# Performance work log

Hardware: AMD Instinct MI355X
Metric: run time of the kernel (lower is better)

## Reference

```python
import jax, jax.numpy as jnp
import numpy as np

N_NODES = 100000
N_EDGES = 1600000
HIDDEN = 128
MAX_DEG = 64
EPS = 1e-6


def setup_inputs() -> dict:
    key = jax.random.key(0)
    ks = jax.random.split(key, 6)
    x = jax.random.randint(ks[0], (N_NODES,), 0, MAX_DEG + 1)
    edge_index = jax.random.randint(ks[1], (2, N_EDGES), 0, N_NODES)
    edge_weight = jax.random.uniform(ks[2], (N_EDGES,), dtype=jnp.float32)
    emb = jax.random.normal(ks[3], (MAX_DEG + 1, HIDDEN), dtype=jnp.float32)
    # 5 GraphNorms in application order: emb_gn, conv0.gn, gns[0], conv1.gn, gns[1]
    gn_weight = jax.random.uniform(ks[4], (5, HIDDEN), dtype=jnp.float32)
    gn_bias = jnp.zeros((5, HIDDEN), dtype=jnp.float32)
    gn_mean_scale = jax.random.uniform(ks[5], (5, HIDDEN), dtype=jnp.float32)
    return {"x": x, "edge_index": edge_index, "edge_weight": edge_weight,
            "emb": emb, "gn_weight": gn_weight, "gn_bias": gn_bias,
            "gn_mean_scale": gn_mean_scale}


def _graphnorm(h, w, b, ms):
    # GLASS GraphNorm over the whole node set (single-graph batch)
    mean = jnp.mean(h, axis=0)              # [D]
    out = h - mean * ms                     # [N,D]
    std = jnp.sqrt(jnp.mean(out * out, axis=0) + EPS)
    return w * out / std + b


def reference(x, edge_index, edge_weight, emb, gn_weight, gn_bias, gn_mean_scale):
    row, col = edge_index[0], edge_index[1]
    n = N_NODES
    # mean-aggregated normalized adjacency (buildAdj, aggr='mean')
    deg = jax.ops.segment_sum(edge_weight, row, num_segments=n)
    deg = jnp.where(deg < 0.5, deg + 1.0, deg)
    w_norm = edge_weight / deg[row]         # [E]

    def spmm(h):
        # (adj @ h)[i] = sum_{e: row[e]=i} w_norm[e] * h[col[e]]
        return jax.ops.segment_sum(h[col] * w_norm[:, None], row, num_segments=n)

    # input embedding + emb_gn (dropout is identity in eval mode)
    h = emb[x]                              # [N, HIDDEN]
    h = _graphnorm(h, gn_weight[0], gn_bias[0], gn_mean_scale[0])
    # layer 0: GLASSConv (adj @ h -> gn) then outer gns[0] and ReLU
    h = spmm(h)
    h = _graphnorm(h, gn_weight[1], gn_bias[1], gn_mean_scale[1])
    h = _graphnorm(h, gn_weight[2], gn_bias[2], gn_mean_scale[2])
    h = jax.nn.relu(h)
    # layer 1 (last conv) then final gns[-1]; jk=False -> take last
    h = spmm(h)
    h = _graphnorm(h, gn_weight[3], gn_bias[3], gn_mean_scale[3])
    h = _graphnorm(h, gn_weight[4], gn_bias[4], gn_mean_scale[4])
    return h
```

## Files before the change

kernel.cpp:

```cpp
#include <hip/hip_runtime.h>

#define HID 128
#define EPSF 1e-6f

__device__ inline unsigned f2bf(float f) {
  unsigned u = __float_as_uint(f);
  return (u + 0x7fffu + ((u >> 16) & 1u)) >> 16;
}

__global__ void k_hist(const int* __restrict__ x, int n, int* __restrict__ hist) {
  __shared__ int lh[65];
  int t = threadIdx.x;
  if (t < 65) lh[t] = 0;
  __syncthreads();
  for (int i = blockIdx.x * blockDim.x + t; i < n; i += gridDim.x * blockDim.x)
    atomicAdd(&lh[x[i]], 1);
  __syncthreads();
  if (t < 65 && lh[t]) atomicAdd(&hist[t], lh[t]);
}

__global__ void k_cnt(const int* __restrict__ row, int e, int* __restrict__ cnt) {
  for (int i = blockIdx.x * blockDim.x + threadIdx.x; i < e; i += gridDim.x * blockDim.x)
    atomicAdd(&cnt[row[i]], 1);
}

__global__ void k_scan_partial(const int* __restrict__ cnt, int n, int* __restrict__ bsum) {
  __shared__ int sh[256];
  int t = threadIdx.x;
  int base = blockIdx.x * 2048 + t * 8;
  int s = 0;
#pragma unroll
  for (int j = 0; j < 8; ++j) { int idx = base + j; if (idx < n) s += cnt[idx]; }
  sh[t] = s; __syncthreads();
  for (int off = 128; off > 0; off >>= 1) {
    if (t < off) sh[t] += sh[t + off];
    __syncthreads();
  }
  if (t == 0) bsum[blockIdx.x] = sh[0];
}

__global__ void k_scan_bsum(int* __restrict__ bsum, int nb) {
  if (threadIdx.x == 0 && blockIdx.x == 0) {
    int acc = 0;
    for (int i = 0; i < nb; ++i) { int v = bsum[i]; bsum[i] = acc; acc += v; }
  }
}

__global__ void k_scan_final(const int* __restrict__ cnt, int n, const int* __restrict__ bsum,
                             int* __restrict__ rowptr, int* __restrict__ cursor) {
  __shared__ int sh[256];
  int t = threadIdx.x;
  int base = blockIdx.x * 2048 + t * 8;
  int v[8]; int s = 0;
#pragma unroll
  for (int j = 0; j < 8; ++j) { int idx = base + j; v[j] = (idx < n) ? cnt[idx] : 0; s += v[j]; }
  sh[t] = s; __syncthreads();
  for (int off = 1; off < 256; off <<= 1) {
    int val = (t >= off) ? sh[t - off] : 0;
    __syncthreads();
    sh[t] += val;
    __syncthreads();
  }
  int off0 = bsum[blockIdx.x] + sh[t] - s;
#pragma unroll
  for (int j = 0; j < 8; ++j) {
    int idx = base + j;
    if (idx < n) { rowptr[idx] = off0; cursor[idx] = off0; off0 += v[j]; }
  }
}

__global__ void k_scatter(const int* __restrict__ row, const int* __restrict__ col,
                          const float* __restrict__ ew, const int* __restrict__ x, int e,
                          int* __restrict__ cursor, int2* __restrict__ sedge) {
  for (int i = blockIdx.x * blockDim.x + threadIdx.x; i < e; i += gridDim.x * blockDim.x) {
    int r = row[i];
    int c = col[i];
    int xc = x[c];
    int pos = atomicAdd(&cursor[r], 1);
    sedge[pos] = make_int2(c | (xc << 17), __float_as_int(ew[i]));
  }
}

__global__ void k_gn0(const float* __restrict__ emb, const int* __restrict__ hist,
                      const float* __restrict__ gw, const float* __restrict__ gb,
                      const float* __restrict__ gms, float invN,
                      float* __restrict__ emb1) {
  int d = threadIdx.x;
  float s = 0.f, s2 = 0.f;
  for (int k = 0; k < 65; ++k) {
    float v = emb[k * HID + d];
    float c = (float)hist[k];
    s += c * v; s2 += c * v * v;
  }
  float m = s * invN, E2 = s2 * invN;
  float ms0 = gms[d], w0 = gw[d], b0 = gb[d];
  float sh = m * ms0;
  float a = w0 / sqrtf(E2 - 2.f * sh * m + sh * sh + EPSF);
  float c = b0 - a * sh;
  for (int k = 0; k < 65; ++k) emb1[k * HID + d] = fmaf(a, emb[k * HID + d], c);
}

__global__ void k_gnchain(const float* __restrict__ gsum, const float* __restrict__ gsq,
                          float invN, const float* __restrict__ gw, const float* __restrict__ gb,
                          const float* __restrict__ gms, int i1, int i2,
                          float* __restrict__ A, float* __restrict__ C) {
  int d = threadIdx.x;
  float m = gsum[d] * invN, E2 = gsq[d] * invN;
  float ms1 = gms[i1 * HID + d], w1 = gw[i1 * HID + d], b1 = gb[i1 * HID + d];
  float sh1 = m * ms1;
  float a1 = w1 / sqrtf(E2 - 2.f * sh1 * m + sh1 * sh1 + EPSF);
  float c1 = b1 - a1 * sh1;
  float m2 = a1 * m + c1;
  float E2b = a1 * a1 * E2 + 2.f * a1 * c1 * m + c1 * c1;
  float ms2 = gms[i2 * HID + d], w2 = gw[i2 * HID + d], b2 = gb[i2 * HID + d];
  float sh2 = m2 * ms2;
  float a2 = w2 / sqrtf(E2b - 2.f * sh2 * m2 + sh2 * sh2 + EPSF);
  float c2 = b2 - a2 * sh2;
  A[d] = a2 * a1;
  C[d] = a2 * c1 + c2;
}

__global__ __launch_bounds__(256) void k_spmm1(
    const int* __restrict__ rowptr, const int2* __restrict__ sedge,
    const float* __restrict__ emb1, int n, int nwaves,
    unsigned* __restrict__ h2b, float* __restrict__ gsum, float* __restrict__ gsq) {
  __shared__ float lemb[65 * HID];
  __shared__ float red[2][4][64][2];
  int t = threadIdx.x;
  for (int i = t; i < 65 * HID; i += 256) lemb[i] = emb1[i];
  __syncthreads();
  int l = t & 63, wv = t >> 6;
  int gwid = blockIdx.x * 4 + wv;
  float ps0 = 0, ps1 = 0, q0 = 0, q1 = 0;
  for (int node = gwid; node < n; node += nwaves) {
    int nd = __builtin_amdgcn_readfirstlane(node);
    int p0 = rowptr[nd], p1 = rowptr[nd + 1];
    float wsum = 0.f, a0 = 0.f, a1 = 0.f;
    int p = p0;
    int nfull = p0 + ((p1 - p0) & ~7);
    for (; p < nfull; p += 8) {
      int2 b[8];
#pragma unroll
      for (int k = 0; k < 8; ++k) b[k] = sedge[p + k];
#pragma unroll
      for (int k = 0; k < 8; ++k) {
        int xc = b[k].x >> 17;
        float w = __int_as_float(b[k].y);
        const float2 v = *(const float2*)&lemb[xc * HID + l * 2];
        wsum += w;
        a0 = fmaf(w, v.x, a0);
        a1 = fmaf(w, v.y, a1);
      }
    }
    for (; p < p1; ++p) {
      int2 b = sedge[p];
      int xc = b.x >> 17;
      float w = __int_as_float(b.y);
      const float2 v = *(const float2*)&lemb[xc * HID + l * 2];
      wsum += w;
      a0 = fmaf(w, v.x, a0);
      a1 = fmaf(w, v.y, a1);
    }
    float d = (wsum < 0.5f) ? wsum + 1.0f : wsum;
    float invd = 1.0f / d;
    a0 *= invd; a1 *= invd;
    h2b[(size_t)node * (HID / 2) + l] = f2bf(a0) | (f2bf(a1) << 16);
    ps0 += a0; ps1 += a1; q0 += a0 * a0; q1 += a1 * a1;
  }
  red[0][wv][l][0] = ps0; red[0][wv][l][1] = ps1;
  red[1][wv][l][0] = q0;  red[1][wv][l][1] = q1;
  __syncthreads();
  if (wv == 0) {
    float s0 = 0, s1 = 0, t0 = 0, t1 = 0;
#pragma unroll
    for (int k = 0; k < 4; ++k) {
      s0 += red[0][k][l][0]; s1 += red[0][k][l][1];
      t0 += red[1][k][l][0]; t1 += red[1][k][l][1];
    }
    atomicAdd(&gsum[l * 2], s0); atomicAdd(&gsum[l * 2 + 1], s1);
    atomicAdd(&gsq[l * 2], t0);  atomicAdd(&gsq[l * 2 + 1], t1);
  }
}

__global__ __launch_bounds__(256) void k_spmm2(
    const int* __restrict__ rowptr, const int2* __restrict__ sedge,
    const unsigned* __restrict__ h2b,
    const float* __restrict__ A, const float* __restrict__ C,
    int n, int nwaves, float* __restrict__ out,
    float* __restrict__ gsum, float* __restrict__ gsq) {
  __shared__ float red[2][4][64][2];
  int t = threadIdx.x;
  int l = t & 63, wv = t >> 6;
  int gwid = blockIdx.x * 4 + wv;
  float A0 = A[l * 2], A1 = A[l * 2 + 1], C0 = C[l * 2], C1 = C[l * 2 + 1];
  float ps0 = 0, ps1 = 0, q0 = 0, q1 = 0;
  for (int node = gwid; node < n; node += nwaves) {
    int nd = __builtin_amdgcn_readfirstlane(node);
    int p0 = rowptr[nd], p1 = rowptr[nd + 1];
    float wsum = 0.f, a0 = 0.f, a1 = 0.f;
    int cntf = (p1 - p0) >> 3;
    int p = p0;
    int2 b[8], nb[8];
    if (cntf) {
#pragma unroll
      for (int k = 0; k < 8; ++k) b[k] = sedge[p + k];
    }
    for (int it = 0; it < cntf; ++it) {
      unsigned u[8];
#pragma unroll
      for (int k = 0; k < 8; ++k) {
        int c = b[k].x & 0x1FFFF;
        u[k] = h2b[(size_t)c * (HID / 2) + l];
      }
      p += 8;
      if (it + 1 < cntf) {
#pragma unroll
        for (int k = 0; k < 8; ++k) nb[k] = sedge[p + k];
      }
#pragma unroll
      for (int k = 0; k < 8; ++k) {
        float w = __int_as_float(b[k].y);
        wsum += w;
        float h0 = __uint_as_float(u[k] << 16);
        float h1 = __uint_as_float(u[k] & 0xFFFF0000u);
        a0 = fmaf(w, fmaxf(fmaf(A0, h0, C0), 0.f), a0);
        a1 = fmaf(w, fmaxf(fmaf(A1, h1, C1), 0.f), a1);
      }
#pragma unroll
      for (int k = 0; k < 8; ++k) b[k] = nb[k];
    }
    for (; p < p1; ++p) {
      int2 e = sedge[p];
      int c = e.x & 0x1FFFF;
      unsigned uu = h2b[(size_t)c * (HID / 2) + l];
      float w = __int_as_float(e.y);
      wsum += w;
      float h0 = __uint_as_float(uu << 16);
      float h1 = __uint_as_float(uu & 0xFFFF0000u);
      a0 = fmaf(w, fmaxf(fmaf(A0, h0, C0), 0.f), a0);
      a1 = fmaf(w, fmaxf(fmaf(A1, h1, C1), 0.f), a1);
    }
    float d = (wsum < 0.5f) ? wsum + 1.0f : wsum;
    float invd = 1.0f / d;
    a0 *= invd; a1 *= invd;
    *(float2*)&out[(size_t)node * HID + l * 2] = make_float2(a0, a1);
    ps0 += a0; ps1 += a1; q0 += a0 * a0; q1 += a1 * a1;
  }
  red[0][wv][l][0] = ps0; red[0][wv][l][1] = ps1;
  red[1][wv][l][0] = q0;  red[1][wv][l][1] = q1;
  __syncthreads();
  if (wv == 0) {
    float s0 = 0, s1 = 0, t0 = 0, t1 = 0;
#pragma unroll
    for (int k = 0; k < 4; ++k) {
      s0 += red[0][k][l][0]; s1 += red[0][k][l][1];
      t0 += red[1][k][l][0]; t1 += red[1][k][l][1];
    }
    atomicAdd(&gsum[l * 2], s0); atomicAdd(&gsum[l * 2 + 1], s1);
    atomicAdd(&gsq[l * 2], t0);  atomicAdd(&gsq[l * 2 + 1], t1);
  }
}

__global__ void k_final(float* __restrict__ out, const float* __restrict__ A,
                        const float* __restrict__ C, int n) {
  __shared__ float la[HID], lc[HID];
  if (threadIdx.x < HID) { la[threadIdx.x] = A[threadIdx.x]; lc[threadIdx.x] = C[threadIdx.x]; }
  __syncthreads();
  int total = n * 32;
  for (int i = blockIdx.x * blockDim.x + threadIdx.x; i < total; i += gridDim.x * blockDim.x) {
    float4 v = *(float4*)(out + (size_t)i * 4);
    int cg = (i & 31) * 4;
    v.x = fmaf(la[cg + 0], v.x, lc[cg + 0]);
    v.y = fmaf(la[cg + 1], v.y, lc[cg + 1]);
    v.z = fmaf(la[cg + 2], v.z, lc[cg + 2]);
    v.w = fmaf(la[cg + 3], v.w, lc[cg + 3]);
    *(float4*)(out + (size_t)i * 4) = v;
  }
}

extern "C" void kernel_launch(void* const* d_in, const int* in_sizes, int n_in,
                              void* d_out, int out_size, void* d_ws, size_t ws_size,
                              hipStream_t stream) {
  const int* x = (const int*)d_in[0];
  const int* ei = (const int*)d_in[1];
  const float* ew = (const float*)d_in[2];
  const float* emb = (const float*)d_in[3];
  const float* gw = (const float*)d_in[4];
  const float* gb = (const float*)d_in[5];
  const float* gms = (const float*)d_in[6];
  float* out = (float*)d_out;

  const int n = in_sizes[0];
  const int e = in_sizes[1] / 2;
  const int* row = ei;
  const int* col = ei + e;

  float* wsf = (float*)d_ws;
  size_t o = 0;
  auto alloc = [&](size_t elems) -> size_t { size_t r = o; o += ((elems + 31) & ~(size_t)31); return r; };
  size_t cnt_o = alloc(n + 1);
  size_t hist_o = alloc(65);
  size_t sum2_o = alloc(HID), sq2_o = alloc(HID), sum4_o = alloc(HID), sq4_o = alloc(HID);
  size_t zero_end = o;
  size_t A12_o = alloc(HID), C12_o = alloc(HID), A34_o = alloc(HID), C34_o = alloc(HID);
  size_t rowptr_o = alloc(n + 1);
  size_t cursor_o = alloc(n + 1);
  size_t bsum_o = alloc(64);
  size_t emb1_o = alloc(65 * HID);
  size_t sedge_o = alloc((size_t)e * 2);
  size_t h2b_o = alloc((size_t)n * HID / 2);

  int* cnt = (int*)(wsf + cnt_o);
  int* hist = (int*)(wsf + hist_o);
  float* sum2 = wsf + sum2_o; float* sq2 = wsf + sq2_o;
  float* sum4 = wsf + sum4_o; float* sq4 = wsf + sq4_o;
  float* A12 = wsf + A12_o; float* C12 = wsf + C12_o;
  float* A34 = wsf + A34_o; float* C34 = wsf + C34_o;
  int* rowptr = (int*)(wsf + rowptr_o);
  int* cursor = (int*)(wsf + cursor_o);
  int* bsum = (int*)(wsf + bsum_o);
  float* emb1 = wsf + emb1_o;
  int2* sedge = (int2*)(wsf + sedge_o);
  unsigned* h2b = (unsigned*)(wsf + h2b_o);

  const float invN = 1.0f / (float)n;
  const int nblk = 2048;
  const int nwaves = nblk * 4;

  hipMemsetAsync(d_ws, 0, zero_end * sizeof(float), stream);
  k_hist<<<256, 256, 0, stream>>>(x, n, hist);
  k_cnt<<<2048, 256, 0, stream>>>(row, e, cnt);
  int nb = (n + 1 + 2047) / 2048;
  k_scan_partial<<<nb, 256, 0, stream>>>(cnt, n + 1, bsum);
  k_scan_bsum<<<1, 64, 0, stream>>>(bsum, nb);
  k_scan_final<<<nb, 256, 0, stream>>>(cnt, n + 1, bsum, rowptr, cursor);
  k_scatter<<<2048, 256, 0, stream>>>(row, col, ew, x, e, cursor, sedge);
  k_gn0<<<1, HID, 0, stream>>>(emb, hist, gw, gb, gms, invN, emb1);
  k_spmm1<<<nblk, 256, 0, stream>>>(rowptr, sedge, emb1, n, nwaves, h2b, sum2, sq2);
  k_gnchain<<<1, HID, 0, stream>>>(sum2, sq2, invN, gw, gb, gms, 1, 2, A12, C12);
  k_spmm2<<<nblk, 256, 0, stream>>>(rowptr, sedge, h2b, A12, C12, n, nwaves, out, sum4, sq4);
  k_gnchain<<<1, HID, 0, stream>>>(sum4, sq4, invN, gw, gb, gms, 3, 4, A34, C34);
  k_final<<<2048, 256, 0, stream>>>(out, A34, C34, n);
}
```

Baseline: 567.9 us.

## Software-pipeline SpMM gathers, bf16 embedding table, fuse hist/count, unroll scatter

Merges the histogram and row-count kernels into one launch. The edge scatter is unrolled by four so several independent loads and atomics are in flight per thread. The normalised embedding table is stored as packed bf16 in global memory instead of fp32 in LDS, which drops the per-block 33KB LDS fill and raises occupancy but adds rounding error to layer 0. Both SpMM kernels get a double-buffered pipeline over 8-edge chunks, prefetch of the next node's rowptr, a vectorised remainder path, and a launch_bounds occupancy hint, at the cost of higher register pressure.

```diff
diff --git a/kernel.cpp b/kernel.cpp
--- a/kernel.cpp
+++ b/kernel.cpp
@@ -8,20 +8,17 @@
   return (u + 0x7fffu + ((u >> 16) & 1u)) >> 16;
 }
 
-__global__ void k_hist(const int* __restrict__ x, int n, int* __restrict__ hist) {
+__global__ void k_histcnt(const int* __restrict__ x, int n, const int* __restrict__ row,
+                          int e, int* __restrict__ hist, int* __restrict__ cnt) {
   __shared__ int lh[65];
   int t = threadIdx.x;
   if (t < 65) lh[t] = 0;
   __syncthreads();
-  for (int i = blockIdx.x * blockDim.x + t; i < n; i += gridDim.x * blockDim.x)
-    atomicAdd(&lh[x[i]], 1);
+  int tid = blockIdx.x * blockDim.x + t, stride = gridDim.x * blockDim.x;
+  for (int i = tid; i < e; i += stride) atomicAdd(&cnt[row[i]], 1);
+  for (int i = tid; i < n; i += stride) atomicAdd(&lh[x[i]], 1);
   __syncthreads();
   if (t < 65 && lh[t]) atomicAdd(&hist[t], lh[t]);
-}
-
-__global__ void k_cnt(const int* __restrict__ row, int e, int* __restrict__ cnt) {
-  for (int i = blockIdx.x * blockDim.x + threadIdx.x; i < e; i += gridDim.x * blockDim.x)
-    atomicAdd(&cnt[row[i]], 1);
 }
 
 __global__ void k_scan_partial(const int* __restrict__ cnt, int n, int* __restrict__ bsum) {
@@ -69,35 +66,53 @@
   }
 }
 
-__global__ void k_scatter(const int* __restrict__ row, const int* __restrict__ col,
-                          const float* __restrict__ ew, const int* __restrict__ x, int e,
-                          int* __restrict__ cursor, int2* __restrict__ sedge) {
-  for (int i = blockIdx.x * blockDim.x + threadIdx.x; i < e; i += gridDim.x * blockDim.x) {
-    int r = row[i];
-    int c = col[i];
-    int xc = x[c];
-    int pos = atomicAdd(&cursor[r], 1);
-    sedge[pos] = make_int2(c | (xc << 17), __float_as_int(ew[i]));
+__global__ __launch_bounds__(256) void k_scatter(
+    const int* __restrict__ row, const int* __restrict__ col,
+    const float* __restrict__ ew, const int* __restrict__ x, int e,
+    int* __restrict__ cursor, int2* __restrict__ sedge) {
+  int tid = blockIdx.x * blockDim.x + threadIdx.x;
+  int stride = gridDim.x * blockDim.x;
+  for (int i0 = tid; i0 < e; i0 += stride * 4) {
+    int r[4], c[4], xc[4], idx[4]; float w[4]; bool valid[4];
+#pragma unroll
+    for (int k = 0; k < 4; ++k) {
+      int i = i0 + k * stride; valid[k] = (i < e);
+      if (valid[k]) { r[k] = row[i]; c[k] = col[i]; w[k] = ew[i]; }
+    }
+#pragma unroll
+    for (int k = 0; k < 4; ++k) if (valid[k]) xc[k] = x[c[k]];
+#pragma unroll
+    for (int k = 0; k < 4; ++k) if (valid[k]) idx[k] = atomicAdd(&cursor[r[k]], 1);
+#pragma unroll
+    for (int k = 0; k < 4; ++k)
+      if (valid[k]) sedge[idx[k]] = make_int2(c[k] | (xc[k] << 17), __float_as_int(w[k]));
   }
 }
 
 __global__ void k_gn0(const float* __restrict__ emb, const int* __restrict__ hist,
                       const float* __restrict__ gw, const float* __restrict__ gb,
                       const float* __restrict__ gms, float invN,
-                      float* __restrict__ emb1) {
-  int d = threadIdx.x;
-  float s = 0.f, s2 = 0.f;
+                      unsigned* __restrict__ emb1b) {
+  int t = threadIdx.x;
+  int d0 = t * 2, d1 = t * 2 + 1;
+  float s0 = 0, s20 = 0, s1 = 0, s21 = 0;
   for (int k = 0; k < 65; ++k) {
-    float v = emb[k * HID + d];
     float c = (float)hist[k];
-    s += c * v; s2 += c * v * v;
-  }
-  float m = s * invN, E2 = s2 * invN;
-  float ms0 = gms[d], w0 = gw[d], b0 = gb[d];
-  float sh = m * ms0;
-  float a = w0 / sqrtf(E2 - 2.f * sh * m + sh * sh + EPSF);
-  float c = b0 - a * sh;
-  for (int k = 0; k < 65; ++k) emb1[k * HID + d] = fmaf(a, emb[k * HID + d], c);
+    float v0 = emb[k * HID + d0], v1 = emb[k * HID + d1];
+    s0 += c * v0; s20 += c * v0 * v0;
+    s1 += c * v1; s21 += c * v1 * v1;
+  }
+  float m0 = s0 * invN, E20 = s20 * invN;
+  float m1 = s1 * invN, E21 = s21 * invN;
+  float sh0 = m0 * gms[d0], sh1 = m1 * gms[d1];
+  float aa0 = gw[d0] / sqrtf(E20 - 2.f * sh0 * m0 + sh0 * sh0 + EPSF);
+  float aa1 = gw[d1] / sqrtf(E21 - 2.f * sh1 * m1 + sh1 * sh1 + EPSF);
+  float cc0 = gb[d0] - aa0 * sh0, cc1 = gb[d1] - aa1 * sh1;
+  for (int k = 0; k < 65; ++k) {
+    float y0 = fmaf(aa0, emb[k * HID + d0], cc0);
+    float y1 = fmaf(aa1, emb[k * HID + d1], cc1);
+    emb1b[k * (HID / 2) + t] = f2bf(y0) | (f2bf(y1) << 16);
+  }
 }
 
 __global__ void k_gnchain(const float* __restrict__ gsum, const float* __restrict__ gsq,
@@ -120,55 +135,94 @@
   C[d] = a2 * c1 + c2;
 }
 
-__global__ __launch_bounds__(256) void k_spmm1(
+#define LOADB(B) { _Pragma("unroll") for (int k = 0; k < 8; ++k) B[k] = sedge[p + k]; p += 8; }
+#define WCOPY(W, B) { _Pragma("unroll") for (int k = 0; k < 8; ++k) W[k] = __int_as_float(B[k].y); }
+
+__global__ __launch_bounds__(256, 8) void k_spmm1(
     const int* __restrict__ rowptr, const int2* __restrict__ sedge,
-    const float* __restrict__ emb1, int n, int nwaves,
+    const unsigned* __restrict__ emb1b, int n, int nwaves,
     unsigned* __restrict__ h2b, float* __restrict__ gsum, float* __restrict__ gsq) {
-  __shared__ float lemb[65 * HID];
   __shared__ float red[2][4][64][2];
   int t = threadIdx.x;
-  for (int i = t; i < 65 * HID; i += 256) lemb[i] = emb1[i];
-  __syncthreads();
   int l = t & 63, wv = t >> 6;
   int gwid = blockIdx.x * 4 + wv;
-  float ps0 = 0, ps1 = 0, q0 = 0, q1 = 0;
+  float ps0 = 0, ps1 = 0, q0s = 0, q1s = 0;
+
+#define GATHER1(U, B) { _Pragma("unroll") for (int k = 0; k < 8; ++k) \
+    U[k] = emb1b[(unsigned)(B[k].x >> 17) * (HID / 2) + l]; }
+#define COMP1(U, W) { _Pragma("unroll") for (int k = 0; k < 8; ++k) { \
+    float w = W[k]; wsum += w; \
+    float h0 = __uint_as_float(U[k] << 16); \
+    float h1 = __uint_as_float(U[k] & 0xFFFF0000u); \
+    a0 = fmaf(w, h0, a0); a1 = fmaf(w, h1, a1); } }
+
+  int p0 = 0, p1 = 0;
+  if (gwid < n) { p0 = rowptr[gwid]; p1 = rowptr[gwid + 1]; }
   for (int node = gwid; node < n; node += nwaves) {
-    int nd = __builtin_amdgcn_readfirstlane(node);
-    int p0 = rowptr[nd], p1 = rowptr[nd + 1];
+    int nxt = node + nwaves;
+    int q0 = 0, q1 = 0;
+    if (nxt < n) { q0 = rowptr[nxt]; q1 = rowptr[nxt + 1]; }
+    int m = p1 - p0;
+    int cnt8 = m >> 3;
+    int p = p0;
     float wsum = 0.f, a0 = 0.f, a1 = 0.f;
-    int p = p0;
-    int nfull = p0 + ((p1 - p0) & ~7);
-    for (; p < nfull; p += 8) {
-      int2 b[8];
-#pragma unroll
-      for (int k = 0; k < 8; ++k) b[k] = sedge[p + k];
-#pragma unroll
-      for (int k = 0; k < 8; ++k) {
-        int xc = b[k].x >> 17;
-        float w = __int_as_float(b[k].y);
-        const float2 v = *(const float2*)&lemb[xc * HID + l * 2];
-        wsum += w;
-        a0 = fmaf(w, v.x, a0);
-        a1 = fmaf(w, v.y, a1);
-      }
-    }
-    for (; p < p1; ++p) {
-      int2 b = sedge[p];
-      int xc = b.x >> 17;
-      float w = __int_as_float(b.y);
-      const float2 v = *(const float2*)&lemb[xc * HID + l * 2];
-      wsum += w;
-      a0 = fmaf(w, v.x, a0);
-      a1 = fmaf(w, v.y, a1);
+    if (cnt8 >= 2) {
+      int2 bA[8], bB[8]; unsigned uA[8], uB[8]; float wA[8], wB[8];
+      LOADB(bA); LOADB(bB);
+      GATHER1(uA, bA); WCOPY(wA, bA);
+      int i = 0;
+      for (; i + 3 < cnt8; i += 2) {
+        GATHER1(uB, bB); WCOPY(wB, bB);
+        LOADB(bA);
+        COMP1(uA, wA);
+        GATHER1(uA, bA); WCOPY(wA, bA);
+        LOADB(bB);
+        COMP1(uB, wB);
+      }
+      if (cnt8 - i == 3) {
+        GATHER1(uB, bB); WCOPY(wB, bB);
+        LOADB(bA);
+        COMP1(uA, wA);
+        GATHER1(uA, bA); WCOPY(wA, bA);
+        COMP1(uB, wB);
+        COMP1(uA, wA);
+      } else {
+        GATHER1(uB, bB); WCOPY(wB, bB);
+        COMP1(uA, wA);
+        COMP1(uB, wB);
+      }
+    } else if (cnt8 == 1) {
+      int2 bA[8]; unsigned uA[8]; float wA[8];
+      LOADB(bA);
+      GATHER1(uA, bA); WCOPY(wA, bA);
+      COMP1(uA, wA);
+    }
+    int r = m & 7;
+    if (r) {
+      p = p0 + (cnt8 << 3);
+      int2 bR[8]; unsigned uR[8];
+#pragma unroll
+      for (int k = 0; k < 8; ++k) if (k < r) bR[k] = sedge[p + k];
+#pragma unroll
+      for (int k = 0; k < 8; ++k) if (k < r)
+        uR[k] = emb1b[(unsigned)(bR[k].x >> 17) * (HID / 2) + l];
+#pragma unroll
+      for (int k = 0; k < 8; ++k) if (k < r) {
+        float w = __int_as_float(bR[k].y); wsum += w;
+        float h0 = __uint_as_float(uR[k] << 16);
+        float h1 = __uint_as_float(uR[k] & 0xFFFF0000u);
+        a0 = fmaf(w, h0, a0); a1 = fmaf(w, h1, a1);
+      }
     }
     float d = (wsum < 0.5f) ? wsum + 1.0f : wsum;
     float invd = 1.0f / d;
     a0 *= invd; a1 *= invd;
     h2b[(size_t)node * (HID / 2) + l] = f2bf(a0) | (f2bf(a1) << 16);
-    ps0 += a0; ps1 += a1; q0 += a0 * a0; q1 += a1 * a1;
+    ps0 += a0; ps1 += a1; q0s += a0 * a0; q1s += a1 * a1;
+    p0 = q0; p1 = q1;
   }
   red[0][wv][l][0] = ps0; red[0][wv][l][1] = ps1;
-  red[1][wv][l][0] = q0;  red[1][wv][l][1] = q1;
+  red[1][wv][l][0] = q0s; red[1][wv][l][1] = q1s;
   __syncthreads();
   if (wv == 0) {
     float s0 = 0, s1 = 0, t0 = 0, t1 = 0;
@@ -182,7 +236,7 @@
   }
 }
 
-__global__ __launch_bounds__(256) void k_spmm2(
+__global__ __launch_bounds__(256, 8) void k_spmm2(
     const int* __restrict__ rowptr, const int2* __restrict__ sedge,
     const unsigned* __restrict__ h2b,
     const float* __restrict__ A, const float* __restrict__ C,
@@ -193,61 +247,85 @@
   int l = t & 63, wv = t >> 6;
   int gwid = blockIdx.x * 4 + wv;
   float A0 = A[l * 2], A1 = A[l * 2 + 1], C0 = C[l * 2], C1 = C[l * 2 + 1];
-  float ps0 = 0, ps1 = 0, q0 = 0, q1 = 0;
+  float ps0 = 0, ps1 = 0, q0s = 0, q1s = 0;
+
+#define GATHER2(U, B) { _Pragma("unroll") for (int k = 0; k < 8; ++k) \
+    U[k] = h2b[(size_t)(B[k].x & 0x1FFFF) * (HID / 2) + l]; }
+#define COMP2(U, W) { _Pragma("unroll") for (int k = 0; k < 8; ++k) { \
+    float w = W[k]; wsum += w; \
+    float h0 = __uint_as_float(U[k] << 16); \
+    float h1 = __uint_as_float(U[k] & 0xFFFF0000u); \
+    a0 = fmaf(w, fmaxf(fmaf(A0, h0, C0), 0.f), a0); \
+    a1 = fmaf(w, fmaxf(fmaf(A1, h1, C1), 0.f), a1); } }
+
+  int p0 = 0, p1 = 0;
+  if (gwid < n) { p0 = rowptr[gwid]; p1 = rowptr[gwid + 1]; }
   for (int node = gwid; node < n; node += nwaves) {
-    int nd = __builtin_amdgcn_readfirstlane(node);
-    int p0 = rowptr[nd], p1 = rowptr[nd + 1];
+    int nxt = node + nwaves;
+    int q0 = 0, q1 = 0;
+    if (nxt < n) { q0 = rowptr[nxt]; q1 = rowptr[nxt + 1]; }
+    int m = p1 - p0;
+    int cnt8 = m >> 3;
+    int p = p0;
     float wsum = 0.f, a0 = 0.f, a1 = 0.f;
-    int cntf = (p1 - p0) >> 3;
-    int p = p0;
-    int2 b[8], nb[8];
-    if (cntf) {
-#pragma unroll
-      for (int k = 0; k < 8; ++k) b[k] = sedge[p + k];
-    }
-    for (int it = 0; it < cntf; ++it) {
-      unsigned u[8];
-#pragma unroll
-      for (int k = 0; k < 8; ++k) {
-        int c = b[k].x & 0x1FFFF;
-        u[k] = h2b[(size_t)c * (HID / 2) + l];
-      }
-      p += 8;
-      if (it + 1 < cntf) {
-#pragma unroll
-        for (int k = 0; k < 8; ++k) nb[k] = sedge[p + k];
-      }
-#pragma unroll
-      for (int k = 0; k < 8; ++k) {
-        float w = __int_as_float(b[k].y);
-        wsum += w;
-        float h0 = __uint_as_float(u[k] << 16);
-        float h1 = __uint_as_float(u[k] & 0xFFFF0000u);
+    if (cnt8 >= 2) {
+      int2 bA[8], bB[8]; unsigned uA[8], uB[8]; float wA[8], wB[8];
+      LOADB(bA); LOADB(bB);
+      GATHER2(uA, bA); WCOPY(wA, bA);
+      int i = 0;
+      for (; i + 3 < cnt8; i += 2) {
+        GATHER2(uB, bB); WCOPY(wB, bB);
+        LOADB(bA);
+        COMP2(uA, wA);
+        GATHER2(uA, bA); WCOPY(wA, bA);
+        LOADB(bB);
+        COMP2(uB, wB);
+      }
+      if (cnt8 - i == 3) {
+        GATHER2(uB, bB); WCOPY(wB, bB);
+        LOADB(bA);
+        COMP2(uA, wA);
+        GATHER2(uA, bA); WCOPY(wA, bA);
+        COMP2(uB, wB);
+        COMP2(uA, wA);
+      } else {
+        GATHER2(uB, bB); WCOPY(wB, bB);
+        COMP2(uA, wA);
+        COMP2(uB, wB);
+      }
+    } else if (cnt8 == 1) {
+      int2 bA[8]; unsigned uA[8]; float wA[8];
+      LOADB(bA);
+      GATHER2(uA, bA); WCOPY(wA, bA);
+      COMP2(uA, wA);
+    }
+    int r = m & 7;
+    if (r) {
+      p = p0 + (cnt8 << 3);
+      int2 bR[8]; unsigned uR[8];
+#pragma unroll
+      for (int k = 0; k < 8; ++k) if (k < r) bR[k] = sedge[p + k];
+#pragma unroll
+      for (int k = 0; k < 8; ++k) if (k < r)
+        uR[k] = h2b[(size_t)(bR[k].x & 0x1FFFF) * (HID / 2) + l];
+#pragma unroll
+      for (int k = 0; k < 8; ++k) if (k < r) {
+        float w = __int_as_float(bR[k].y); wsum += w;
+        float h0 = __uint_as_float(uR[k] << 16);
+        float h1 = __uint_as_float(uR[k] & 0xFFFF0000u);
         a0 = fmaf(w, fmaxf(fmaf(A0, h0, C0), 0.f), a0);
         a1 = fmaf(w, fmaxf(fmaf(A1, h1, C1), 0.f), a1);
       }
-#pragma unroll
-      for (int k = 0; k < 8; ++k) b[k] = nb[k];
-    }
-    for (; p < p1; ++p) {
-      int2 e = sedge[p];
-      int c = e.x & 0x1FFFF;
-      unsigned uu = h2b[(size_t)c * (HID / 2) + l];
-      float w = __int_as_float(e.y);
-      wsum += w;
-      float h0 = __uint_as_float(uu << 16);
-      float h1 = __uint_as_float(uu & 0xFFFF0000u);
-      a0 = fmaf(w, fmaxf(fmaf(A0, h0, C0), 0.f), a0);
-      a1 = fmaf(w, fmaxf(fmaf(A1, h1, C1), 0.f), a1);
     }
     float d = (wsum < 0.5f) ? wsum + 1.0f : wsum;
     float invd = 1.0f / d;
     a0 *= invd; a1 *= invd;
     *(float2*)&out[(size_t)node * HID + l * 2] = make_float2(a0, a1);
-    ps0 += a0; ps1 += a1; q0 += a0 * a0; q1 += a1 * a1;
+    ps0 += a0; ps1 += a1; q0s += a0 * a0; q1s += a1 * a1;
+    p0 = q0; p1 = q1;
   }
   red[0][wv][l][0] = ps0; red[0][wv][l][1] = ps1;
-  red[1][wv][l][0] = q0;  red[1][wv][l][1] = q1;
+  red[1][wv][l][0] = q0s; red[1][wv][l][1] = q1s;
   __syncthreads();
   if (wv == 0) {
     float s0 = 0, s1 = 0, t0 = 0, t1 = 0;
@@ -306,7 +384,7 @@
   size_t rowptr_o = alloc(n + 1);
   size_t cursor_o = alloc(n + 1);
   size_t bsum_o = alloc(64);
-  size_t emb1_o = alloc(65 * HID);
+  size_t emb1b_o = alloc(65 * HID / 2);
   size_t sedge_o = alloc((size_t)e * 2);
   size_t h2b_o = alloc((size_t)n * HID / 2);
 
@@ -319,7 +397,7 @@
   int* rowptr = (int*)(wsf + rowptr_o);
   int* cursor = (int*)(wsf + cursor_o);
   int* bsum = (int*)(wsf + bsum_o);
-  float* emb1 = wsf + emb1_o;
+  unsigned* emb1b = (unsigned*)(wsf + emb1b_o);
   int2* sedge = (int2*)(wsf + sedge_o);
   unsigned* h2b = (unsigned*)(wsf + h2b_o);
 
@@ -328,15 +406,14 @@
   const int nwaves = nblk * 4;
 
   hipMemsetAsync(d_ws, 0, zero_end * sizeof(float), stream);
-  k_hist<<<256, 256, 0, stream>>>(x, n, hist);
-  k_cnt<<<2048, 256, 0, stream>>>(row, e, cnt);
+  k_histcnt<<<2048, 256, 0, stream>>>(x, n, row, e, hist, cnt);
   int nb = (n + 1 + 2047) / 2048;
   k_scan_partial<<<nb, 256, 0, stream>>>(cnt, n + 1, bsum);
   k_scan_bsum<<<1, 64, 0, stream>>>(bsum, nb);
   k_scan_final<<<nb, 256, 0, stream>>>(cnt, n + 1, bsum, rowptr, cursor);
   k_scatter<<<2048, 256, 0, stream>>>(row, col, ew, x, e, cursor, sedge);
-  k_gn0<<<1, HID, 0, stream>>>(emb, hist, gw, gb, gms, invN, emb1);
-  k_spmm1<<<nblk, 256, 0, stream>>>(rowptr, sedge, emb1, n, nwaves, h2b, sum2, sq2);
+  k_gn0<<<1, 64, 0, stream>>>(emb, hist, gw, gb, gms, invN, emb1b);
+  k_spmm1<<<nblk, 256, 0, stream>>>(rowptr, sedge, emb1b, n, nwaves, h2b, sum2, sq2);
   k_gnchain<<<1, HID, 0, stream>>>(sum2, sq2, invN, gw, gb, gms, 1, 2, A12, C12);
   k_spmm2<<<nblk, 256, 0, stream>>>(rowptr, sedge, h2b, A12, C12, n, nwaves, out, sum4, sq4);
   k_gnchain<<<1, HID, 0, stream>>>(sum4, sq4, invN, gw, gb, gms, 3, 4, A34, C34);
```

Measured after the change: 1.073 ms. 1.89x slower.
